# Performance work log

Hardware: AMD Instinct MI355X
Metric: run time of the kernel (lower is better)

The kernel has to match this reference:

```python
import jax, jax.numpy as jnp
import numpy as np

T, IN_SZ, OUT_SZ = 512, 1024, 1024
INIT_TAU = 2.0   # sig_tau = sigmoid(init_tau) is the leak factor
V_TH = 1.0


def setup_inputs() -> dict:
    key = jax.random.key(0)
    k1, k2 = jax.random.split(key)
    x_seq = jax.random.normal(k1, (T, IN_SZ), jnp.float32)
    kernel = jax.random.normal(k2, (IN_SZ, OUT_SZ), jnp.float32) / np.float32(np.sqrt(IN_SZ))
    u0 = jnp.zeros((OUT_SZ,), jnp.float32)
    E0 = jnp.zeros((IN_SZ, OUT_SZ), jnp.float32)  # eligibility trace, same shape as kernel
    return {"x_seq": x_seq, "kernel": kernel, "u0": u0, "E0": E0}


def reference(x_seq, kernel, u0, E0):
    # Forward pass of the OSTL-wrapped spiking cell over a sequence.
    # Primal path (f): LIF dynamics with soft reset; E is not touched in primal.
    sig_tau = jax.nn.sigmoid(jnp.float32(INIT_TAU))
    vth = jnp.float32(V_TH)

    def body(u, x):
        u_new = sig_tau * u + x @ kernel          # [OUT_SZ]
        s = (u_new > vth).astype(x.dtype)          # heaviside spike
        u_out = u_new - s * vth                    # soft reset
        return u_out, s

    u_final, spikes = jax.lax.scan(body, u0, x_seq)  # spikes: [T, OUT_SZ]
    return spikes, u_final
```

## Files before the change

kernel.cpp:

```cpp
#include <hip/hip_runtime.h>
#include <stdint.h>


#define T_STEPS 512
#define IN_SZ   1024
#define OUT_SZ  1024

#define BM 128
#define BN 128
#define BK 32
#define KSPLIT 8
#define KCHUNK (IN_SZ / KSPLIT)
#define NITER  (KCHUNK / BK)

typedef __attribute__((address_space(1))) const void gvoid;
typedef __attribute__((address_space(3))) void lvoid;

__global__ __launch_bounds__(256) void ostl_gemm_splitk(const float* __restrict__ X,
                                                        const float* __restrict__ W,
                                                        float* __restrict__ P) {
    __shared__ float As[2][BK][BM];
    __shared__ float Bs[2][BK * BN];

    const int tid = threadIdx.x;
    const int tx = tid & 15;
    const int ty = tid >> 4;
    const int n0 = blockIdx.x * BN;
    const int m0 = blockIdx.y * BM;
    const int kc = blockIdx.z;
    const int kb = kc * KCHUNK;

    const int am = tid >> 1;
    const int ak = (tid & 1) * 16;
    const int wv = tid >> 6;
    const int ln = tid & 63;

    const float* Arow = X + (size_t)(m0 + am) * IN_SZ + kb + ak;

    float4 areg[4];

    #pragma unroll
    for (int q = 0; q < 4; ++q)
        areg[q] = *reinterpret_cast<const float4*>(Arow + q * 4);
    #pragma unroll
    for (int j = 0; j < 4; ++j) {
        const int i = wv * 4 + j;
        const float* src = W + (size_t)(kb + 2 * i + (ln >> 5)) * OUT_SZ + n0 + (ln & 31) * 4;
        __builtin_amdgcn_global_load_lds((gvoid*)src, (lvoid*)&Bs[0][i * 256], 16, 0, 0);
    }
    {
        float t[16];
        #pragma unroll
        for (int q = 0; q < 4; ++q) *reinterpret_cast<float4*>(&t[q * 4]) = areg[q];
        #pragma unroll
        for (int c = 0; c < 16; ++c) As[0][ak + c][am] = t[c];
    }
    __syncthreads();

    float acc[8][8];
    #pragma unroll
    for (int r = 0; r < 8; ++r)
        #pragma unroll
        for (int c = 0; c < 8; ++c) acc[r][c] = 0.f;

    #pragma unroll 1
    for (int it = 0; it < NITER; ++it) {
        const int cur = it & 1;
        const int nxt = cur ^ 1;

        if (it < NITER - 1) {
            const int kbase = kb + (it + 1) * BK;
            #pragma unroll
            for (int j = 0; j < 4; ++j) {
                const int i = wv * 4 + j;
                const float* src = W + (size_t)(kbase + 2 * i + (ln >> 5)) * OUT_SZ + n0 + (ln & 31) * 4;
                __builtin_amdgcn_global_load_lds((gvoid*)src, (lvoid*)&Bs[nxt][i * 256], 16, 0, 0);
            }
            #pragma unroll
            for (int q = 0; q < 4; ++q)
                areg[q] = *reinterpret_cast<const float4*>(Arow + (it + 1) * BK + q * 4);
        }

        #pragma unroll 8
        for (int k = 0; k < BK; ++k) {
            const float4 a0 = *reinterpret_cast<const float4*>(&As[cur][k][ty * 8]);
            const float4 a1 = *reinterpret_cast<const float4*>(&As[cur][k][ty * 8 + 4]);
            const float4 b0 = *reinterpret_cast<const float4*>(&Bs[cur][k * BN + tx * 4]);
            const float4 b1 = *reinterpret_cast<const float4*>(&Bs[cur][k * BN + tx * 4 + 64]);
            const float av[8] = {a0.x, a0.y, a0.z, a0.w, a1.x, a1.y, a1.z, a1.w};
            const float bv[8] = {b0.x, b0.y, b0.z, b0.w, b1.x, b1.y, b1.z, b1.w};
            #pragma unroll
            for (int r = 0; r < 8; ++r)
                #pragma unroll
                for (int c = 0; c < 8; ++c)
                    acc[r][c] = fmaf(av[r], bv[c], acc[r][c]);
        }

        if (it < NITER - 1) {
            float t[16];
            #pragma unroll
            for (int q = 0; q < 4; ++q) *reinterpret_cast<float4*>(&t[q * 4]) = areg[q];
            #pragma unroll
            for (int c = 0; c < 16; ++c) As[nxt][ak + c][am] = t[c];
            __syncthreads();
        }
    }

    float* Pb = P + (size_t)kc * T_STEPS * OUT_SZ + (size_t)(m0 + ty * 8) * OUT_SZ + n0;
    #pragma unroll
    for (int r = 0; r < 8; ++r) {
        *reinterpret_cast<float4*>(&Pb[(size_t)r * OUT_SZ + tx * 4]) =
            make_float4(acc[r][0], acc[r][1], acc[r][2], acc[r][3]);
        *reinterpret_cast<float4*>(&Pb[(size_t)r * OUT_SZ + tx * 4 + 64]) =
            make_float4(acc[r][4], acc[r][5], acc[r][6], acc[r][7]);
    }
}

__device__ inline float4 f4add(float4 a, float4 b) {
    return make_float4(a.x + b.x, a.y + b.y, a.z + b.z, a.w + b.w);
}

__global__ __launch_bounds__(256) void ostl_reduce8(const float* __restrict__ P,
                                                    float* __restrict__ Y) {
    const size_t idx = ((size_t)blockIdx.x * 256 + threadIdx.x) * 4;
    float4 s[8];
    #pragma unroll
    for (int c = 0; c < 8; ++c)
        s[c] = *reinterpret_cast<const float4*>(P + (size_t)c * T_STEPS * OUT_SZ + idx);
    const float4 t0 = f4add(s[0], s[1]);
    const float4 t1 = f4add(s[2], s[3]);
    const float4 t2 = f4add(s[4], s[5]);
    const float4 t3 = f4add(s[6], s[7]);
    *reinterpret_cast<float4*>(Y + idx) = f4add(f4add(t0, t1), f4add(t2, t3));
}

__global__ __launch_bounds__(64) void ostl_scan_wave(const float* __restrict__ u0,
                                                     const float* __restrict__ Y,
                                                     float* __restrict__ Sout,
                                                     float* __restrict__ u_final) {
    const int j = blockIdx.x;
    const int l = threadIdx.x;

    const float  sig_f   = (float)0.8807970779778823;
    const double sig_tau = (double)sig_f;

    float y[8];
    #pragma unroll
    for (int q = 0; q < 8; ++q)
        y[q] = Y[(size_t)(q * 64 + l) * OUT_SZ + j];

    double u = (double)u0[j];
    float spk[8];

    #pragma unroll
    for (int q = 0; q < 8; ++q) {
        #pragma unroll
        for (int i = 0; i < 64; ++i) {
            const float  yv = __shfl(y[q], i, 64);
            const double un = fma(sig_tau, u, (double)yv);
            const double us = un - 1.0;
            const bool   sp = un > 1.0;
            const float  s  = sp ? 1.0f : 0.0f;
            if (i == l) spk[q] = s;
            u = sp ? us : un;
        }
    }

    #pragma unroll
    for (int q = 0; q < 8; ++q)
        Sout[(size_t)(q * 64 + l) * OUT_SZ + j] = spk[q];
    if (l == 0) u_final[j] = (float)u;
}

extern "C" void kernel_launch(void* const* d_in, const int* in_sizes, int n_in,
                              void* d_out, int out_size, void* d_ws, size_t ws_size,
                              hipStream_t stream) {
    const float* x_seq  = (const float*)d_in[0];
    const float* kernel = (const float*)d_in[1];
    const float* u0     = (const float*)d_in[2];

    float* out      = (float*)d_out;
    float* spikes   = out;
    float* u_final  = out + (size_t)T_STEPS * OUT_SZ;

    float* partials = (float*)d_ws;
    float* yb       = partials + (size_t)KSPLIT * T_STEPS * OUT_SZ;

    dim3 ggrid(OUT_SZ / BN, T_STEPS / BM, KSPLIT);
    ostl_gemm_splitk<<<ggrid, dim3(256), 0, stream>>>(x_seq, kernel, partials);

    ostl_reduce8<<<dim3((T_STEPS * OUT_SZ / 4) / 256), dim3(256), 0, stream>>>(partials, yb);

    ostl_scan_wave<<<dim3(OUT_SZ), dim3(64), 0, stream>>>(u0, yb, spikes, u_final);
}
```

Before: 115.5 us.

## Pack spikes as bitmasks in scan and expand with coalesced separate kernel

The scan kernel now broadcasts each step's input with readlane instead of a shuffle, prefetches the next 64-step chunk of Y inside a non-unrolled outer loop, and records spikes as per-lane bitmasks rather than scattered float stores. A new expand kernel turns the bitmasks into the float spike matrix with coalesced float4 row writes. The aim is to replace the strided column stores and the shuffle cost in the serial scan, at the price of one extra kernel launch and an extra workspace buffer.

```diff
diff --git a/kernel.cpp b/kernel.cpp
--- a/kernel.cpp
+++ b/kernel.cpp
@@ -134,42 +134,54 @@
     *reinterpret_cast<float4*>(Y + idx) = f4add(f4add(t0, t1), f4add(t2, t3));
 }
 
-__global__ __launch_bounds__(64) void ostl_scan_wave(const float* __restrict__ u0,
-                                                     const float* __restrict__ Y,
-                                                     float* __restrict__ Sout,
-                                                     float* __restrict__ u_final) {
+__global__ __launch_bounds__(64) void ostl_scan_rl(const float* __restrict__ u0,
+                                                   const float* __restrict__ Y,
+                                                   unsigned* __restrict__ Bits,
+                                                   float* __restrict__ u_final) {
     const int j = blockIdx.x;
     const int l = threadIdx.x;
 
     const float  sig_f   = (float)0.8807970779778823;
     const double sig_tau = (double)sig_f;
 
-    float y[8];
-    #pragma unroll
-    for (int q = 0; q < 8; ++q)
-        y[q] = Y[(size_t)(q * 64 + l) * OUT_SZ + j];
-
     double u = (double)u0[j];
-    float spk[8];
-
-    #pragma unroll
+    unsigned sbits = 0u;
+
+    float ycur = Y[(size_t)l * OUT_SZ + j];
+    #pragma unroll 1
     for (int q = 0; q < 8; ++q) {
+        float ynext = 0.f;
+        if (q < 7)
+            ynext = Y[(size_t)((q + 1) * 64 + l) * OUT_SZ + j];
+        const unsigned qbit = 1u << q;
         #pragma unroll
         for (int i = 0; i < 64; ++i) {
-            const float  yv = __shfl(y[q], i, 64);
+            const float  yv = __int_as_float(
+                __builtin_amdgcn_readlane(__float_as_int(ycur), i));
             const double un = fma(sig_tau, u, (double)yv);
             const double us = un - 1.0;
             const bool   sp = un > 1.0;
-            const float  s  = sp ? 1.0f : 0.0f;
-            if (i == l) spk[q] = s;
+            sbits |= (i == l && sp) ? qbit : 0u;
             u = sp ? us : un;
         }
-    }
-
-    #pragma unroll
-    for (int q = 0; q < 8; ++q)
-        Sout[(size_t)(q * 64 + l) * OUT_SZ + j] = spk[q];
+        ycur = ynext;
+    }
+    Bits[(size_t)j * 64 + l] = sbits;
     if (l == 0) u_final[j] = (float)u;
+}
+
+__global__ __launch_bounds__(256) void ostl_expand(const unsigned* __restrict__ Bits,
+                                                   float* __restrict__ S) {
+    const int t = blockIdx.x;
+    const int c = t & 63;
+    const int q = t >> 6;
+    const int j4 = threadIdx.x * 4;
+    float4 v;
+    v.x = (float)((Bits[(size_t)(j4 + 0) * 64 + c] >> q) & 1u);
+    v.y = (float)((Bits[(size_t)(j4 + 1) * 64 + c] >> q) & 1u);
+    v.z = (float)((Bits[(size_t)(j4 + 2) * 64 + c] >> q) & 1u);
+    v.w = (float)((Bits[(size_t)(j4 + 3) * 64 + c] >> q) & 1u);
+    *reinterpret_cast<float4*>(&S[(size_t)t * OUT_SZ + j4]) = v;
 }
 
 extern "C" void kernel_launch(void* const* d_in, const int* in_sizes, int n_in,
@@ -183,13 +195,16 @@
     float* spikes   = out;
     float* u_final  = out + (size_t)T_STEPS * OUT_SZ;
 
-    float* partials = (float*)d_ws;
-    float* yb       = partials + (size_t)KSPLIT * T_STEPS * OUT_SZ;
+    float*    partials = (float*)d_ws;
+    float*    yb       = partials + (size_t)KSPLIT * T_STEPS * OUT_SZ;
+    unsigned* bits     = (unsigned*)(yb + (size_t)T_STEPS * OUT_SZ);
 
     dim3 ggrid(OUT_SZ / BN, T_STEPS / BM, KSPLIT);
     ostl_gemm_splitk<<<ggrid, dim3(256), 0, stream>>>(x_seq, kernel, partials);
 
     ostl_reduce8<<<dim3((T_STEPS * OUT_SZ / 4) / 256), dim3(256), 0, stream>>>(partials, yb);
 
-    ostl_scan_wave<<<dim3(OUT_SZ), dim3(64), 0, stream>>>(u0, yb, spikes, u_final);
-}
+    ostl_scan_rl<<<dim3(OUT_SZ), dim3(64), 0, stream>>>(u0, yb, bits, u_final);
+
+    ostl_expand<<<dim3(T_STEPS), dim3(256), 0, stream>>>(bits, spikes);
+}
```

Measured after the change: 107.6 us. -6.8%, faster.
